# Performance work log

Hardware: AMD Instinct MI355X
Metric: run time of the kernel (lower is better)

## Reference

```python
import jax, jax.numpy as jnp
import numpy as np
from functools import partial

STRIDES = (8, 16, 32)
SCORE_THRESH = 0.3
NMS_THRESH = 0.5
TOPK = 500          # fixed pre-NMS candidate count (jit-friendly substitute for boolean masking)
CLASS_OFFSET = 1e4  # offset boxes per class so cross-class IoU == 0 -> per-class NMS


def _decode(cls, reg, obj, stride):
    # cls [B,C,H,W], reg [B,4,H,W], obj [B,1,H,W]
    B, C, H, W = cls.shape
    yv, xv = jnp.meshgrid(jnp.arange(H, dtype=cls.dtype), jnp.arange(W, dtype=cls.dtype), indexing='ij')
    scores = jax.nn.sigmoid(obj) * jax.nn.sigmoid(cls)          # [B,C,H,W]
    dx, dy, dw, dh = reg[:, 0], reg[:, 1], reg[:, 2], reg[:, 3]
    cx = (xv + jax.nn.sigmoid(dx)) * stride
    cy = (yv + jax.nn.sigmoid(dy)) * stride
    w = jnp.exp(dw) * stride
    h = jnp.exp(dh) * stride
    boxes = jnp.stack([cx - w / 2, cy - h / 2, cx + w / 2, cy + h / 2], axis=-1)  # [B,H,W,4]
    return boxes.reshape(B, H * W, 4), scores.reshape(B, C, H * W).transpose(0, 2, 1)


def _pairwise_iou(boxes):
    # boxes [B,K,4] xyxy -> iou [B,K,K]
    area = (boxes[..., 2] - boxes[..., 0]) * (boxes[..., 3] - boxes[..., 1])
    x1 = jnp.maximum(boxes[:, :, None, 0], boxes[:, None, :, 0])
    y1 = jnp.maximum(boxes[:, :, None, 1], boxes[:, None, :, 1])
    x2 = jnp.minimum(boxes[:, :, None, 2], boxes[:, None, :, 2])
    y2 = jnp.minimum(boxes[:, :, None, 3], boxes[:, None, :, 3])
    inter = jnp.clip(x2 - x1, 0) * jnp.clip(y2 - y1, 0)
    union = area[:, :, None] + area[:, None, :] - inter
    return inter / (union + 1e-7)


def _greedy_nms(iou, valid):
    # iou [B,K,K], valid [B,K] -> keep [B,K]; greedy over score-sorted order (axis 1)
    B, K = valid.shape
    def step(supp, i):
        keep_i = valid[:, i] & ~supp[:, i]                    # [B]
        supp = supp | (keep_i[:, None] & (iou[:, i, :] >= NMS_THRESH))
        return supp, keep_i
    _, keep_t = jax.lax.scan(step, jnp.zeros((B, K), dtype=bool), jnp.arange(K))
    return keep_t.T  # [B,K]


def _predict(levels):
    boxes_l, scores_l = [], []
    for (c, r, o), s in zip(levels, STRIDES):
        b, sc = _decode(c, r, o, s)
        boxes_l.append(b)
        scores_l.append(sc)
    boxes = jnp.concatenate(boxes_l, axis=1)     # [B,N,4]
    scores = jnp.concatenate(scores_l, axis=1)   # [B,N,C]
    max_scores = scores.max(axis=-1)             # [B,N]
    labels = jnp.argmax(scores, axis=-1)         # [B,N]
    masked = jnp.where(max_scores > SCORE_THRESH, max_scores, -1.0)
    top_scores, idx = jax.lax.top_k(masked, TOPK)                         # sorted desc
    top_boxes = jnp.take_along_axis(boxes, idx[..., None], axis=1)        # [B,K,4]
    top_labels = jnp.take_along_axis(labels, idx, axis=1)                 # [B,K]
    valid = top_scores > SCORE_THRESH
    boxes_off = top_boxes + (top_labels.astype(top_boxes.dtype) * CLASS_OFFSET)[..., None]
    keep = _greedy_nms(_pairwise_iou(boxes_off), valid)                   # [B,K]
    out_boxes = jnp.where(keep[..., None], top_boxes, 0.0)
    out_scores = jnp.where(keep, top_scores, 0.0)
    return out_boxes, out_scores, top_labels, keep


def setup_inputs() -> dict:
    key = jax.random.key(0)
    ks = jax.random.split(key, 9)
    B, C = 64, 2
    shapes = {
        'cls_p3': (B, C, 160, 160), 'reg_p3': (B, 4, 160, 160), 'obj_p3': (B, 1, 160, 160),
        'cls_p4': (B, C, 80, 80),   'reg_p4': (B, 4, 80, 80),   'obj_p4': (B, 1, 80, 80),
        'cls_p5': (B, C, 40, 40),   'reg_p5': (B, 4, 40, 40),   'obj_p5': (B, 1, 40, 40),
    }
    return {name: jax.random.normal(k, shp, dtype=jnp.float32)
            for k, (name, shp) in zip(ks, shapes.items())}


def reference(cls_p3, reg_p3, obj_p3, cls_p4, reg_p4, obj_p4, cls_p5, reg_p5, obj_p5):
    levels = [(cls_p3, reg_p3, obj_p3), (cls_p4, reg_p4, obj_p4), (cls_p5, reg_p5, obj_p5)]
    return _predict(levels)
```

## Files before the change

kernel.cpp:

```cpp
#include <hip/hip_runtime.h>
#include <hip/hip_bf16.h>
#include <stdint.h>

#define NB 64
#define NA 33600
#define NK 500
#define HW3 25600
#define HW4 6400
#define HW5 1600
#define OFF4 25600
#define OFF5 32000
#define NBIN 2048
#define CAP 2048
#define NA4 8400
#define MROWS 512

typedef unsigned int u32;
typedef unsigned long long u64;

__device__ __forceinline__ float sigf(float x) { return 1.0f / (1.0f + expf(-x)); }

__device__ __forceinline__ u32 f2key(float f) {
  u32 u = __float_as_uint(f);
  return (u & 0x80000000u) ? ~u : (u | 0x80000000u);
}
__device__ __forceinline__ float key2f(u32 k) {
  u32 u = (k & 0x80000000u) ? (k ^ 0x80000000u) : ~k;
  return __uint_as_float(u);
}
__device__ __forceinline__ int bin_of(float s) {
  int b = (int)(s * 2048.0f);
  return b > 2047 ? 2047 : b;
}
__device__ __forceinline__ u32 mkkey(float o, float c0, float c1) {
  float so = sigf(o);
  float s = fmaxf(so * sigf(c0), so * sigf(c1));
  float masked = (s > 0.3f) ? s : -1.0f;
  return f2key(masked);
}
__device__ __forceinline__ u64 uniform64(u64 v) {
  u32 lo = (u32)__builtin_amdgcn_readfirstlane((int)(u32)v);
  u32 hi = (u32)__builtin_amdgcn_readfirstlane((int)(u32)(v >> 32));
  return ((u64)hi << 32) | lo;
}

__global__ __launch_bounds__(256) void k_score(
    const float* __restrict__ cls3, const float* __restrict__ obj3,
    const float* __restrict__ cls4, const float* __restrict__ obj4,
    const float* __restrict__ cls5, const float* __restrict__ obj5,
    uint4* __restrict__ keys4)
{
  int b = blockIdx.y;
  int i4 = blockIdx.x * 256 + threadIdx.x;
  if (i4 >= NA4) return;
  const float* cls; const float* obj; int p4, HW;
  if (i4 < 6400)      { cls = cls3; obj = obj3; p4 = i4;        HW = HW3; }
  else if (i4 < 8000) { cls = cls4; obj = obj4; p4 = i4 - 6400; HW = HW4; }
  else                { cls = cls5; obj = obj5; p4 = i4 - 8000; HW = HW5; }
  float4 o  = reinterpret_cast<const float4*>(obj + (size_t)b * HW)[p4];
  float4 c0 = reinterpret_cast<const float4*>(cls + (size_t)(b * 2) * HW)[p4];
  float4 c1 = reinterpret_cast<const float4*>(cls + (size_t)(b * 2 + 1) * HW)[p4];
  uint4 kv;
  kv.x = mkkey(o.x, c0.x, c1.x);
  kv.y = mkkey(o.y, c0.y, c1.y);
  kv.z = mkkey(o.z, c0.z, c1.z);
  kv.w = mkkey(o.w, c0.w, c1.w);
  keys4[(size_t)b * NA4 + i4] = kv;
}

__global__ __launch_bounds__(1024) void k_topk(
    const u32* __restrict__ keys,
    const float* __restrict__ cls3, const float* __restrict__ obj3, const float* __restrict__ reg3,
    const float* __restrict__ cls4, const float* __restrict__ obj4, const float* __restrict__ reg4,
    const float* __restrict__ cls5, const float* __restrict__ obj5, const float* __restrict__ reg5,
    float* __restrict__ top_score,
    float4* __restrict__ boxes, float4* __restrict__ boxesoff,
    float* __restrict__ out_labels)
{
  int b = blockIdx.x, tid = threadIdx.x;
  __shared__ u32 hist[NBIN];
  __shared__ u32 part[256];
  __shared__ u64 cand[CAP];
  __shared__ int idx_lds[NK];
  __shared__ u32 lcnt;
  __shared__ int sh_p;
  __shared__ u32 sh_R;
  __shared__ int sh_digit;
  __shared__ u32 sh_cnt;

  for (int i = tid; i < NBIN; i += 1024) hist[i] = 0;
  if (tid < NK) idx_lds[tid] = 0;
  if (tid == 0) { lcnt = 0; }
  __syncthreads();

  const u32* kb = keys + (size_t)b * NA;
  const uint4* kb4 = reinterpret_cast<const uint4*>(kb);

  for (int i4 = tid; i4 < NA4; i4 += 1024) {
    uint4 kv = kb4[i4];
    u32 ks[4] = {kv.x, kv.y, kv.z, kv.w};
#pragma unroll
    for (int c = 0; c < 4; ++c) {
      float s = key2f(ks[c]);
      if (s > 0.3f) atomicAdd(&hist[bin_of(s)], 1u);
    }
  }
  __syncthreads();
  if (tid < 256) {
    u32 s8 = 0;
#pragma unroll
    for (int k = 0; k < 8; ++k) s8 += hist[tid * 8 + k];
    part[tid] = s8;
  }
  __syncthreads();
  for (int off = 1; off < 256; off <<= 1) {
    u32 add = 0;
    if (tid < 256 && tid + off < 256) add = part[tid + off];
    __syncthreads();
    if (tid < 256) part[tid] += add;
    __syncthreads();
  }
  if (tid == 0 && part[0] < NK) sh_p = -1;
  if (tid < 256) {
    u32 S = part[tid];
    u32 Snext = (tid == 255) ? 0u : part[tid + 1];
    if (S >= NK && Snext < NK) {
      u32 run = Snext;
      int p = tid * 8;
      for (int k = 7; k >= 0; --k) {
        run += hist[tid * 8 + k];
        if (run >= NK) { p = tid * 8 + k; break; }
      }
      sh_p = p;
    }
  }
  __syncthreads();
  int p = sh_p;
  bool fail = (p < 0);
  if (!fail) {
    for (int i4 = tid; i4 < NA4; i4 += 1024) {
      uint4 kv = kb4[i4];
      u32 ks[4] = {kv.x, kv.y, kv.z, kv.w};
#pragma unroll
      for (int c = 0; c < 4; ++c) {
        float s = key2f(ks[c]);
        if (s > 0.3f && bin_of(s) >= p) {
          u32 slot = atomicAdd(&lcnt, 1u);
          if (slot < CAP) cand[slot] = ((u64)ks[c] << 16) | (u32)(0xFFFF - (i4 * 4 + c));
        }
      }
    }
    __syncthreads();
    fail = (lcnt > CAP);
  }

  if (!fail) {
    int n = (int)lcnt;
    for (int t = tid; t < n; t += 1024) {
      u64 k = cand[t];
      int rank = 0;
      for (int j = 0; j < n; ++j) rank += (cand[j] > k) ? 1 : 0;
      if (rank < NK) {
        idx_lds[rank] = 0xFFFF - (int)(k & 0xFFFFull);
        top_score[b * NK + rank] = key2f((u32)(k >> 16));
      }
    }
  } else {
    u64 prefix = 0, prefmask = 0;
    u32 R = NK;
    for (int pass = 0; pass < 6; ++pass) {
      int shift = 40 - 8 * pass;
      if (tid < 256) part[tid] = 0;
      __syncthreads();
      for (int i = tid; i < NA; i += 1024) {
        u64 k48 = ((u64)kb[i] << 16) | (u32)(0xFFFF - i);
        if ((k48 & prefmask) == prefix)
          atomicAdd(&part[(u32)(k48 >> shift) & 255u], 1u);
      }
      __syncthreads();
      if (tid < 256) hist[tid] = part[tid];
      __syncthreads();
      for (int off = 1; off < 256; off <<= 1) {
        u32 add = 0;
        if (tid < 256 && tid + off < 256) add = hist[tid + off];
        __syncthreads();
        if (tid < 256) hist[tid] += add;
        __syncthreads();
      }
      if (tid < 256) {
        u32 s = hist[tid];
        u32 snext = (tid == 255) ? 0u : hist[tid + 1];
        if (s >= R && snext < R) { sh_digit = tid; sh_R = R - snext; }
      }
      __syncthreads();
      prefix |= ((u64)sh_digit) << shift;
      R = sh_R;
      prefmask |= 0xFFull << shift;
      __syncthreads();
    }
    if (tid == 0) sh_cnt = 0;
    if (tid < NK) top_score[b * NK + tid] = -1.0f;
    __syncthreads();
    for (int i = tid; i < NA; i += 1024) {
      u64 k48 = ((u64)kb[i] << 16) | (u32)(0xFFFF - i);
      if (k48 >= prefix) {
        u32 slot = atomicAdd(&sh_cnt, 1u);
        if (slot < 512) cand[slot] = k48;
      }
    }
    __syncthreads();
    int n = (sh_cnt < (u32)NK) ? (int)sh_cnt : NK;
    for (int t = tid; t < n; t += 1024) {
      u64 k = cand[t];
      int rank = 0;
      for (int j = 0; j < n; ++j) rank += (cand[j] > k) ? 1 : 0;
      if (rank < NK) {
        idx_lds[rank] = 0xFFFF - (int)(k & 0xFFFFull);
        top_score[b * NK + rank] = key2f((u32)(k >> 16));
      }
    }
  }
  __syncthreads();

  if (tid < NK) {
    int a = idx_lds[tid];
    const float *cls, *obj, *reg; int pos, HW, x, y; float stride;
    if (a < OFF4) {
      cls = cls3; obj = obj3; reg = reg3; pos = a; HW = HW3; stride = 8.0f;
      y = pos / 160; x = pos - y * 160;
    } else if (a < OFF5) {
      cls = cls4; obj = obj4; reg = reg4; pos = a - OFF4; HW = HW4; stride = 16.0f;
      y = pos / 80; x = pos - y * 80;
    } else {
      cls = cls5; obj = obj5; reg = reg5; pos = a - OFF5; HW = HW5; stride = 32.0f;
      y = pos / 40; x = pos - y * 40;
    }
    float dx = reg[(b * 4 + 0) * HW + pos];
    float dy = reg[(b * 4 + 1) * HW + pos];
    float dw = reg[(b * 4 + 2) * HW + pos];
    float dh = reg[(b * 4 + 3) * HW + pos];
    float cx = ((float)x + sigf(dx)) * stride;
    float cy = ((float)y + sigf(dy)) * stride;
    float w = expf(dw) * stride;
    float h = expf(dh) * stride;
    float x1 = cx - w * 0.5f, y1 = cy - h * 0.5f;
    float x2 = cx + w * 0.5f, y2 = cy + h * 0.5f;
    float so = sigf(obj[b * HW + pos]);
    float s0 = so * sigf(cls[(b * 2) * HW + pos]);
    float s1 = so * sigf(cls[(b * 2 + 1) * HW + pos]);
    int label = (s1 > s0) ? 1 : 0;
    float off = (float)label * 10000.0f;
    int t = b * NK + tid;
    boxes[t]    = make_float4(x1, y1, x2, y2);
    boxesoff[t] = make_float4(x1 + off, y1 + off, x2 + off, y2 + off);
    out_labels[t] = (float)label;
  }
}

__global__ __launch_bounds__(256) void k_iou(
    const float4* __restrict__ boxesoff, u64* __restrict__ mask)
{
  int t = blockIdx.x * 256 + threadIdx.x;
  if (t >= NB * NK * 8) return;
  int w = t & 7;
  int bi = t >> 3;
  int b = bi / NK;
  int i = bi - b * NK;
  float4 A = boxesoff[bi];
  float areaA = (A.z - A.x) * (A.w - A.y);
  const float4* base = boxesoff + b * NK;
  int j0 = w * 64;
  int jmax = (NK - j0 < 64) ? (NK - j0) : 64;
  u64 bits = 0;
  for (int jj = 0; jj < jmax; ++jj) {
    float4 Bx = base[j0 + jj];
    float areaB = (Bx.z - Bx.x) * (Bx.w - Bx.y);
    float ix1 = fmaxf(A.x, Bx.x);
    float iy1 = fmaxf(A.y, Bx.y);
    float ix2 = fminf(A.z, Bx.z);
    float iy2 = fminf(A.w, Bx.w);
    float iw = fmaxf(ix2 - ix1, 0.0f);
    float ih = fmaxf(iy2 - iy1, 0.0f);
    float inter = iw * ih;
    float uni = areaA + areaB - inter;
    float iou = inter / (uni + 1e-7f);
    bits |= ((u64)(iou >= 0.5f)) << jj;
  }
  mask[(size_t)b * (MROWS * 8) + (size_t)i * 8 + w] = bits;
}

__global__ __launch_bounds__(64) void k_nms(
    const u64* __restrict__ mask, const float* __restrict__ top_score,
    const float4* __restrict__ boxes,
    float* __restrict__ out_boxes, float* __restrict__ out_scores,
    float* __restrict__ out_keep)
{
  int b = blockIdx.x;
  int lane = threadIdx.x;
  const u64* mb = mask + (size_t)b * (MROWS * 8);

  u64 validw[8];
#pragma unroll
  for (int c = 0; c < 8; ++c) {
    int r = c * 64 + lane;
    float s = (r < NK) ? top_score[b * NK + r] : -1.0f;
    validw[c] = __ballot(s > 0.3f);
  }

  u64 supp[8] = {0, 0, 0, 0, 0, 0, 0, 0};
  u64 keepw[8];
  u64 row[2][8];

  {
    const u64* rp = mb + (size_t)lane * 8;
#pragma unroll
    for (int w = 0; w < 8; ++w) row[0][w] = rp[w];
  }

#pragma unroll
  for (int c = 0; c < 8; ++c) {
    const int cur = c & 1, nxt = cur ^ 1;
    if (c < 7) {
      const u64* rp = mb + (size_t)((c + 1) * 64 + lane) * 8;
#pragma unroll
      for (int w = 0; w < 8; ++w)
        if (w >= c + 1) row[nxt][w] = rp[w];
    }
    u32 rlo = (u32)row[cur][c];
    u32 rhi = (u32)(row[cur][c] >> 32);
    u64 sw = supp[c], vw = validw[c], km = 0;
#pragma unroll
    for (int i = 0; i < 64; ++i) {
      u64 wi = ((u64)(u32)__builtin_amdgcn_readlane(rhi, i) << 32) |
               (u64)(u32)__builtin_amdgcn_readlane(rlo, i);
      u64 bit = 1ull << i;
      if ((vw & bit) && !(sw & bit)) { sw |= wi; km |= bit; }
    }
    keepw[c] = km;
    u64 sel = ((km >> lane) & 1ull) ? ~0ull : 0ull;
#pragma unroll
    for (int w = c + 1; w < 8; ++w) {
      u64 v = row[cur][w] & sel;
#pragma unroll
      for (int off = 1; off < 64; off <<= 1)
        v |= (u64)__shfl_xor((unsigned long long)v, off, 64);
      supp[w] |= uniform64(v);
    }
  }

#pragma unroll
  for (int c = 0; c < 8; ++c) {
    int r = c * 64 + lane;
    if (r < NK) {
      int kp = (int)((keepw[c] >> lane) & 1ull);
      float4 bx = boxes[b * NK + r];
      float s = top_score[b * NK + r];
      float4 ob;
      ob.x = kp ? bx.x : 0.0f;
      ob.y = kp ? bx.y : 0.0f;
      ob.z = kp ? bx.z : 0.0f;
      ob.w = kp ? bx.w : 0.0f;
      reinterpret_cast<float4*>(out_boxes)[b * NK + r] = ob;
      out_scores[b * NK + r] = kp ? s : 0.0f;
      out_keep[b * NK + r]   = kp ? 1.0f : 0.0f;
    }
  }
}

extern "C" void kernel_launch(void* const* d_in, const int* in_sizes, int n_in,
                              void* d_out, int out_size, void* d_ws, size_t ws_size,
                              hipStream_t stream) {
  const float* cls3 = (const float*)d_in[0];
  const float* reg3 = (const float*)d_in[1];
  const float* obj3 = (const float*)d_in[2];
  const float* cls4 = (const float*)d_in[3];
  const float* reg4 = (const float*)d_in[4];
  const float* obj4 = (const float*)d_in[5];
  const float* cls5 = (const float*)d_in[6];
  const float* reg5 = (const float*)d_in[7];
  const float* obj5 = (const float*)d_in[8];

  char* ws = (char*)d_ws;
  u32*    keys      = (u32*)   (ws + 0);
  float*  top_score = (float*) (ws + 8601600);
  float4* boxes     = (float4*)(ws + 8729600);
  float4* boxesoff  = (float4*)(ws + 9241600);
  u64*    mask      = (u64*)   (ws + 9753600);

  float* out        = (float*)d_out;
  float* out_boxes  = out;
  float* out_scores = out + 128000;
  float* out_labels = out + 160000;
  float* out_keep   = out + 192000;

  dim3 gscore((NA4 + 255) / 256, NB);
  k_score<<<gscore, 256, 0, stream>>>(cls3, obj3, cls4, obj4, cls5, obj5, (uint4*)keys);
  k_topk<<<NB, 1024, 0, stream>>>(keys,
      cls3, obj3, reg3, cls4, obj4, reg4, cls5, obj5, reg5,
      top_score, boxes, boxesoff, out_labels);
  k_iou<<<(NB * NK * 8 + 255) / 256, 256, 0, stream>>>(boxesoff, mask);
  k_nms<<<NB, 64, 0, stream>>>(mask, top_score, boxes, out_boxes, out_scores, out_keep);
}
```

Measured before the change: 97.31 us.

## Fuse top-k, IoU mask and greedy NMS into one per-image kernel

Merges the IoU-mask and NMS kernels into the top-k kernel. Scores, boxes and the suppression bitmask now stay in shared memory rather than going through global workspace, and the two extra launches are dropped. The cost is that IoU work is spread over only 64 blocks instead of a wide grid. Shared-memory use per block also rises (about 37KB for the mask alone), which may limit occupancy.

```diff
diff --git a/kernel.cpp b/kernel.cpp
--- a/kernel.cpp
+++ b/kernel.cpp
@@ -13,7 +13,6 @@
 #define NBIN 2048
 #define CAP 2048
 #define NA4 8400
-#define MROWS 512
 
 typedef unsigned int u32;
 typedef unsigned long long u64;
@@ -68,20 +67,24 @@
   keys4[(size_t)b * NA4 + i4] = kv;
 }
 
-__global__ __launch_bounds__(1024) void k_topk(
+__global__ __launch_bounds__(1024) void k_fused(
     const u32* __restrict__ keys,
     const float* __restrict__ cls3, const float* __restrict__ obj3, const float* __restrict__ reg3,
     const float* __restrict__ cls4, const float* __restrict__ obj4, const float* __restrict__ reg4,
     const float* __restrict__ cls5, const float* __restrict__ obj5, const float* __restrict__ reg5,
-    float* __restrict__ top_score,
-    float4* __restrict__ boxes, float4* __restrict__ boxesoff,
-    float* __restrict__ out_labels)
+    float* __restrict__ out_boxes, float* __restrict__ out_scores,
+    float* __restrict__ out_labels, float* __restrict__ out_keep)
 {
   int b = blockIdx.x, tid = threadIdx.x;
   __shared__ u32 hist[NBIN];
   __shared__ u32 part[256];
   __shared__ u64 cand[CAP];
-  __shared__ int idx_lds[NK];
+  __shared__ int idx_lds[512];
+  __shared__ float score_lds[512];
+  __shared__ __align__(16) float4 bo_lds[8 * 65];
+  __shared__ __align__(16) float4 box_lds[NK];
+  __shared__ u64 m_lds[512 * 9];
+  __shared__ u64 keep_share[8];
   __shared__ u32 lcnt;
   __shared__ int sh_p;
   __shared__ u32 sh_R;
@@ -89,8 +92,9 @@
   __shared__ u32 sh_cnt;
 
   for (int i = tid; i < NBIN; i += 1024) hist[i] = 0;
-  if (tid < NK) idx_lds[tid] = 0;
-  if (tid == 0) { lcnt = 0; }
+  if (tid < 512) { idx_lds[tid] = 0; score_lds[tid] = -1.0f; }
+  if (tid < 96) m_lds[(500 + (tid >> 3)) * 9 + (tid & 7)] = 0;
+  if (tid == 0) lcnt = 0;
   __syncthreads();
 
   const u32* kb = keys + (size_t)b * NA;
@@ -162,7 +166,7 @@
       for (int j = 0; j < n; ++j) rank += (cand[j] > k) ? 1 : 0;
       if (rank < NK) {
         idx_lds[rank] = 0xFFFF - (int)(k & 0xFFFFull);
-        top_score[b * NK + rank] = key2f((u32)(k >> 16));
+        score_lds[rank] = key2f((u32)(k >> 16));
       }
     }
   } else {
@@ -199,7 +203,6 @@
       __syncthreads();
     }
     if (tid == 0) sh_cnt = 0;
-    if (tid < NK) top_score[b * NK + tid] = -1.0f;
     __syncthreads();
     for (int i = tid; i < NA; i += 1024) {
       u64 k48 = ((u64)kb[i] << 16) | (u32)(0xFFFF - i);
@@ -216,7 +219,7 @@
       for (int j = 0; j < n; ++j) rank += (cand[j] > k) ? 1 : 0;
       if (rank < NK) {
         idx_lds[rank] = 0xFFFF - (int)(k & 0xFFFFull);
-        top_score[b * NK + rank] = key2f((u32)(k >> 16));
+        score_lds[rank] = key2f((u32)(k >> 16));
       }
     }
   }
@@ -250,120 +253,83 @@
     float s1 = so * sigf(cls[(b * 2 + 1) * HW + pos]);
     int label = (s1 > s0) ? 1 : 0;
     float off = (float)label * 10000.0f;
-    int t = b * NK + tid;
-    boxes[t]    = make_float4(x1, y1, x2, y2);
-    boxesoff[t] = make_float4(x1 + off, y1 + off, x2 + off, y2 + off);
-    out_labels[t] = (float)label;
-  }
-}
-
-__global__ __launch_bounds__(256) void k_iou(
-    const float4* __restrict__ boxesoff, u64* __restrict__ mask)
-{
-  int t = blockIdx.x * 256 + threadIdx.x;
-  if (t >= NB * NK * 8) return;
-  int w = t & 7;
-  int bi = t >> 3;
-  int b = bi / NK;
-  int i = bi - b * NK;
-  float4 A = boxesoff[bi];
-  float areaA = (A.z - A.x) * (A.w - A.y);
-  const float4* base = boxesoff + b * NK;
-  int j0 = w * 64;
-  int jmax = (NK - j0 < 64) ? (NK - j0) : 64;
-  u64 bits = 0;
-  for (int jj = 0; jj < jmax; ++jj) {
-    float4 Bx = base[j0 + jj];
-    float areaB = (Bx.z - Bx.x) * (Bx.w - Bx.y);
-    float ix1 = fmaxf(A.x, Bx.x);
-    float iy1 = fmaxf(A.y, Bx.y);
-    float ix2 = fminf(A.z, Bx.z);
-    float iy2 = fminf(A.w, Bx.w);
-    float iw = fmaxf(ix2 - ix1, 0.0f);
-    float ih = fmaxf(iy2 - iy1, 0.0f);
-    float inter = iw * ih;
-    float uni = areaA + areaB - inter;
-    float iou = inter / (uni + 1e-7f);
-    bits |= ((u64)(iou >= 0.5f)) << jj;
-  }
-  mask[(size_t)b * (MROWS * 8) + (size_t)i * 8 + w] = bits;
-}
-
-__global__ __launch_bounds__(64) void k_nms(
-    const u64* __restrict__ mask, const float* __restrict__ top_score,
-    const float4* __restrict__ boxes,
-    float* __restrict__ out_boxes, float* __restrict__ out_scores,
-    float* __restrict__ out_keep)
-{
-  int b = blockIdx.x;
-  int lane = threadIdx.x;
-  const u64* mb = mask + (size_t)b * (MROWS * 8);
-
-  u64 validw[8];
-#pragma unroll
-  for (int c = 0; c < 8; ++c) {
-    int r = c * 64 + lane;
-    float s = (r < NK) ? top_score[b * NK + r] : -1.0f;
-    validw[c] = __ballot(s > 0.3f);
-  }
-
-  u64 supp[8] = {0, 0, 0, 0, 0, 0, 0, 0};
-  u64 keepw[8];
-  u64 row[2][8];
-
-  {
-    const u64* rp = mb + (size_t)lane * 8;
-#pragma unroll
-    for (int w = 0; w < 8; ++w) row[0][w] = rp[w];
-  }
-
-#pragma unroll
-  for (int c = 0; c < 8; ++c) {
-    const int cur = c & 1, nxt = cur ^ 1;
-    if (c < 7) {
-      const u64* rp = mb + (size_t)((c + 1) * 64 + lane) * 8;
-#pragma unroll
-      for (int w = 0; w < 8; ++w)
-        if (w >= c + 1) row[nxt][w] = rp[w];
-    }
-    u32 rlo = (u32)row[cur][c];
-    u32 rhi = (u32)(row[cur][c] >> 32);
-    u64 sw = supp[c], vw = validw[c], km = 0;
-#pragma unroll
-    for (int i = 0; i < 64; ++i) {
-      u64 wi = ((u64)(u32)__builtin_amdgcn_readlane(rhi, i) << 32) |
-               (u64)(u32)__builtin_amdgcn_readlane(rlo, i);
-      u64 bit = 1ull << i;
-      if ((vw & bit) && !(sw & bit)) { sw |= wi; km |= bit; }
-    }
-    keepw[c] = km;
-    u64 sel = ((km >> lane) & 1ull) ? ~0ull : 0ull;
-#pragma unroll
-    for (int w = c + 1; w < 8; ++w) {
-      u64 v = row[cur][w] & sel;
-#pragma unroll
-      for (int off = 1; off < 64; off <<= 1)
-        v |= (u64)__shfl_xor((unsigned long long)v, off, 64);
-      supp[w] |= uniform64(v);
-    }
-  }
-
-#pragma unroll
-  for (int c = 0; c < 8; ++c) {
-    int r = c * 64 + lane;
-    if (r < NK) {
-      int kp = (int)((keepw[c] >> lane) & 1ull);
-      float4 bx = boxes[b * NK + r];
-      float s = top_score[b * NK + r];
-      float4 ob;
-      ob.x = kp ? bx.x : 0.0f;
-      ob.y = kp ? bx.y : 0.0f;
-      ob.z = kp ? bx.z : 0.0f;
-      ob.w = kp ? bx.w : 0.0f;
-      reinterpret_cast<float4*>(out_boxes)[b * NK + r] = ob;
-      out_scores[b * NK + r] = kp ? s : 0.0f;
-      out_keep[b * NK + r]   = kp ? 1.0f : 0.0f;
-    }
+    box_lds[tid] = make_float4(x1, y1, x2, y2);
+    bo_lds[(tid >> 6) * 65 + (tid & 63)] = make_float4(x1 + off, y1 + off, x2 + off, y2 + off);
+    out_labels[b * NK + tid] = (float)label;
+  }
+  __syncthreads();
+
+  for (int item = tid; item < NK * 8; item += 1024) {
+    int i = item >> 3, w = item & 7;
+    float4 A = bo_lds[(i >> 6) * 65 + (i & 63)];
+    float areaA = (A.z - A.x) * (A.w - A.y);
+    int jmax = (w == 7) ? (NK - 448) : 64;
+    const float4* bp = &bo_lds[w * 65];
+    u64 bits = 0;
+    for (int jj = 0; jj < jmax; ++jj) {
+      float4 Bx = bp[jj];
+      float areaB = (Bx.z - Bx.x) * (Bx.w - Bx.y);
+      float ix1 = fmaxf(A.x, Bx.x);
+      float iy1 = fmaxf(A.y, Bx.y);
+      float ix2 = fminf(A.z, Bx.z);
+      float iy2 = fminf(A.w, Bx.w);
+      float iw = fmaxf(ix2 - ix1, 0.0f);
+      float ih = fmaxf(iy2 - iy1, 0.0f);
+      float inter = iw * ih;
+      float uni = areaA + areaB - inter;
+      float iou = inter / (uni + 1e-7f);
+      bits |= ((u64)(iou >= 0.5f)) << jj;
+    }
+    m_lds[(size_t)i * 9 + w] = bits;
+  }
+  __syncthreads();
+
+  if (tid < 64) {
+    int lane = tid;
+    u64 supp[8] = {0, 0, 0, 0, 0, 0, 0, 0};
+#pragma unroll
+    for (int c = 0; c < 8; ++c) {
+      int r = c * 64 + lane;
+      u64 rw[8];
+#pragma unroll
+      for (int w = 0; w < 8; ++w) rw[w] = m_lds[(size_t)r * 9 + w];
+      u64 vw = __ballot(score_lds[r] > 0.3f);
+      u32 rlo = (u32)rw[c];
+      u32 rhi = (u32)(rw[c] >> 32);
+      u64 sw = supp[c], km = 0;
+#pragma unroll
+      for (int i = 0; i < 64; ++i) {
+        u64 wi = ((u64)(u32)__builtin_amdgcn_readlane(rhi, i) << 32) |
+                 (u64)(u32)__builtin_amdgcn_readlane(rlo, i);
+        u64 bit = 1ull << i;
+        if ((vw & bit) && !(sw & bit)) { sw |= wi; km |= bit; }
+      }
+      if (lane == 0) keep_share[c] = km;
+      u64 sel = ((km >> lane) & 1ull) ? ~0ull : 0ull;
+#pragma unroll
+      for (int w = c + 1; w < 8; ++w) {
+        u64 v = rw[w] & sel;
+#pragma unroll
+        for (int off = 1; off < 64; off <<= 1)
+          v |= (u64)__shfl_xor((unsigned long long)v, off, 64);
+        supp[w] |= uniform64(v);
+      }
+    }
+  }
+  __syncthreads();
+
+  if (tid < NK) {
+    int kp = (int)((keep_share[tid >> 6] >> (tid & 63)) & 1ull);
+    float4 bx = box_lds[tid];
+    float s = score_lds[tid];
+    float4 ob;
+    ob.x = kp ? bx.x : 0.0f;
+    ob.y = kp ? bx.y : 0.0f;
+    ob.z = kp ? bx.z : 0.0f;
+    ob.w = kp ? bx.w : 0.0f;
+    reinterpret_cast<float4*>(out_boxes)[b * NK + tid] = ob;
+    out_scores[b * NK + tid] = kp ? s : 0.0f;
+    out_keep[b * NK + tid]   = kp ? 1.0f : 0.0f;
   }
 }
 
@@ -381,11 +347,7 @@
   const float* obj5 = (const float*)d_in[8];
 
   char* ws = (char*)d_ws;
-  u32*    keys      = (u32*)   (ws + 0);
-  float*  top_score = (float*) (ws + 8601600);
-  float4* boxes     = (float4*)(ws + 8729600);
-  float4* boxesoff  = (float4*)(ws + 9241600);
-  u64*    mask      = (u64*)   (ws + 9753600);
+  u32* keys = (u32*)(ws + 0);
 
   float* out        = (float*)d_out;
   float* out_boxes  = out;
@@ -395,9 +357,7 @@
 
   dim3 gscore((NA4 + 255) / 256, NB);
   k_score<<<gscore, 256, 0, stream>>>(cls3, obj3, cls4, obj4, cls5, obj5, (uint4*)keys);
-  k_topk<<<NB, 1024, 0, stream>>>(keys,
+  k_fused<<<NB, 1024, 0, stream>>>(keys,
       cls3, obj3, reg3, cls4, obj4, reg4, cls5, obj5, reg5,
-      top_score, boxes, boxesoff, out_labels);
-  k_iou<<<(NB * NK * 8 + 255) / 256, 256, 0, stream>>>(boxesoff, mask);
-  k_nms<<<NB, 64, 0, stream>>>(mask, top_score, boxes, out_boxes, out_scores, out_keep);
-}
+      out_boxes, out_scores, out_labels, out_keep);
+}
```

Result: slower. 118.2 us (+21.4%).

## Cache keys in registers and replace rank-count selection with bitonic sort

Applied to the files above, without the earlier changes.

The top-k kernel now loads each batch's keys once into registers and reuses them for both the histogram pass and the candidate-gather pass, removing the second global read. The O(n^2) rank-counting sort of candidates is replaced by a 1024-element bitonic sort in shared memory. The candidate capacity drops from 2048 to 1024, which sends more batches to the slower radix fallback path. Scores are now staged in shared memory and written out together with the boxes.

```diff
diff --git a/kernel.cpp b/kernel.cpp
--- a/kernel.cpp
+++ b/kernel.cpp
@@ -11,8 +11,8 @@
 #define OFF4 25600
 #define OFF5 32000
 #define NBIN 2048
-#define CAP 2048
 #define NA4 8400
+#define LCAP 1024
 #define MROWS 512
 
 typedef unsigned int u32;
@@ -80,8 +80,9 @@
   int b = blockIdx.x, tid = threadIdx.x;
   __shared__ u32 hist[NBIN];
   __shared__ u32 part[256];
-  __shared__ u64 cand[CAP];
+  __shared__ u64 cand[LCAP];
   __shared__ int idx_lds[NK];
+  __shared__ float score_lds[NK];
   __shared__ u32 lcnt;
   __shared__ int sh_p;
   __shared__ u32 sh_R;
@@ -89,16 +90,22 @@
   __shared__ u32 sh_cnt;
 
   for (int i = tid; i < NBIN; i += 1024) hist[i] = 0;
-  if (tid < NK) idx_lds[tid] = 0;
-  if (tid == 0) { lcnt = 0; }
+  if (tid == 0) lcnt = 0;
   __syncthreads();
 
   const u32* kb = keys + (size_t)b * NA;
   const uint4* kb4 = reinterpret_cast<const uint4*>(kb);
 
-  for (int i4 = tid; i4 < NA4; i4 += 1024) {
-    uint4 kv = kb4[i4];
-    u32 ks[4] = {kv.x, kv.y, kv.z, kv.w};
+  uint4 kreg[9];
+#pragma unroll
+  for (int k = 0; k < 9; ++k) {
+    int i4 = tid + k * 1024;
+    kreg[k] = (i4 < NA4) ? kb4[i4] : make_uint4(0u, 0u, 0u, 0u);
+  }
+
+#pragma unroll
+  for (int k = 0; k < 9; ++k) {
+    u32 ks[4] = {kreg[k].x, kreg[k].y, kreg[k].z, kreg[k].w};
 #pragma unroll
     for (int c = 0; c < 4; ++c) {
       float s = key2f(ks[c]);
@@ -138,32 +145,42 @@
   int p = sh_p;
   bool fail = (p < 0);
   if (!fail) {
-    for (int i4 = tid; i4 < NA4; i4 += 1024) {
-      uint4 kv = kb4[i4];
-      u32 ks[4] = {kv.x, kv.y, kv.z, kv.w};
+#pragma unroll
+    for (int k = 0; k < 9; ++k) {
+      int i4 = tid + k * 1024;
+      u32 ks[4] = {kreg[k].x, kreg[k].y, kreg[k].z, kreg[k].w};
 #pragma unroll
       for (int c = 0; c < 4; ++c) {
         float s = key2f(ks[c]);
         if (s > 0.3f && bin_of(s) >= p) {
           u32 slot = atomicAdd(&lcnt, 1u);
-          if (slot < CAP) cand[slot] = ((u64)ks[c] << 16) | (u32)(0xFFFF - (i4 * 4 + c));
+          if (slot < LCAP) cand[slot] = ((u64)ks[c] << 16) | (u32)(0xFFFF - (i4 * 4 + c));
         }
       }
     }
     __syncthreads();
-    fail = (lcnt > CAP);
+    fail = (lcnt > LCAP);
   }
 
   if (!fail) {
-    int n = (int)lcnt;
-    for (int t = tid; t < n; t += 1024) {
-      u64 k = cand[t];
-      int rank = 0;
-      for (int j = 0; j < n; ++j) rank += (cand[j] > k) ? 1 : 0;
-      if (rank < NK) {
-        idx_lds[rank] = 0xFFFF - (int)(k & 0xFFFFull);
-        top_score[b * NK + rank] = key2f((u32)(k >> 16));
-      }
+    for (int i = lcnt + tid; i < LCAP; i += 1024) cand[i] = 0;
+    for (int k = 2; k <= LCAP; k <<= 1) {
+      for (int j = k >> 1; j > 0; j >>= 1) {
+        __syncthreads();
+        if (tid < LCAP / 2) {
+          int i = ((tid & ~(j - 1)) << 1) | (tid & (j - 1));
+          int ixj = i | j;
+          u64 a = cand[i], c2 = cand[ixj];
+          bool dir = ((i & k) == 0);
+          if ((a < c2) == dir) { cand[i] = c2; cand[ixj] = a; }
+        }
+      }
+    }
+    __syncthreads();
+    if (tid < NK) {
+      u64 kk = cand[tid];
+      idx_lds[tid] = 0xFFFF - (int)(kk & 0xFFFFull);
+      score_lds[tid] = key2f((u32)(kk >> 16));
     }
   } else {
     u64 prefix = 0, prefmask = 0;
@@ -199,7 +216,7 @@
       __syncthreads();
     }
     if (tid == 0) sh_cnt = 0;
-    if (tid < NK) top_score[b * NK + tid] = -1.0f;
+    if (tid < NK) { idx_lds[tid] = 0; score_lds[tid] = -1.0f; }
     __syncthreads();
     for (int i = tid; i < NA; i += 1024) {
       u64 k48 = ((u64)kb[i] << 16) | (u32)(0xFFFF - i);
@@ -216,7 +233,7 @@
       for (int j = 0; j < n; ++j) rank += (cand[j] > k) ? 1 : 0;
       if (rank < NK) {
         idx_lds[rank] = 0xFFFF - (int)(k & 0xFFFFull);
-        top_score[b * NK + rank] = key2f((u32)(k >> 16));
+        score_lds[rank] = key2f((u32)(k >> 16));
       }
     }
   }
@@ -254,6 +271,7 @@
     boxes[t]    = make_float4(x1, y1, x2, y2);
     boxesoff[t] = make_float4(x1 + off, y1 + off, x2 + off, y2 + off);
     out_labels[t] = (float)label;
+    top_score[t] = score_lds[tid];
   }
 }
 
```

New measurement: 95.10 us. -2.3%, faster.
